# Kernel tuning notes

Hardware: AMD Instinct MI355X
Metric: run time of the kernel (lower is better)

Reference implementation:

```python
import jax, jax.numpy as jnp
import numpy as np

B, N, D_IN, D_OUT, E = 4, 50000, 128, 128, 800000


def setup_inputs() -> dict:
    key = jax.random.key(0)
    k_x, k_w, k_b, k_r, k_c, k_v = jax.random.split(key, 6)
    stdv = 1.0 / np.sqrt(D_OUT)
    x = jax.random.normal(k_x, (B, N, D_IN), dtype=jnp.float32)
    weight = jax.random.uniform(k_w, (D_IN, D_OUT), jnp.float32, -stdv, stdv)
    bias = jax.random.uniform(k_b, (D_OUT,), jnp.float32, -stdv, stdv)
    adj_rows = jax.random.randint(k_r, (E,), 0, N, dtype=jnp.int32)
    adj_cols = jax.random.randint(k_c, (E,), 0, N, dtype=jnp.int32)
    # positive edge weights (e.g. normalized adjacency values)
    adj_vals = jax.random.uniform(k_v, (E,), jnp.float32) * (1.0 / 16.0)
    edge_index = jnp.stack([adj_rows, adj_cols]).astype(jnp.int64)  # unused (pyg_builtin=False)
    return {"input": x, "weight": weight, "bias": bias,
            "adj_vals": adj_vals, "adj_rows": adj_rows, "adj_cols": adj_cols,
            "edge_index": edge_index}


def reference(input, weight, bias, adj_vals, adj_rows, adj_cols, edge_index):
    # support = input @ W : [B, N, D_OUT]
    support = jnp.einsum('bnd,df->bnf', input, weight)

    # node_repr = sparse adj (COO) @ support, batched == torch.sparse.mm path
    def agg(s):  # s: [N, D_OUT]
        msgs = adj_vals[:, None] * s[adj_cols]          # [E, D_OUT] gather
        return jax.ops.segment_sum(msgs, adj_rows, num_segments=N)  # scatter-add

    node_repr = jax.vmap(agg)(support) + bias           # [B, N, D_OUT]
    # net_norm='none' -> no norm; activation=relu; residual=False; dropout=0
    return jax.nn.relu(node_repr)
```

## Files before the change

### kernel.cpp

```cpp
#include <hip/hip_runtime.h>
#include <hip/hip_bf16.h>

#define BB 4
#define NN 50000
#define DIN 128
#define DOUT 128
#define EE 800000
#define TOTROWS (BB * NN)
#define LDA 136

#define NGB ((TOTROWS + 127) / 128)
#define MAXDEG 64
#define NAB (NN / 4)

typedef unsigned short u16;
typedef unsigned int u32;

using shortx8 = __attribute__((ext_vector_type(8))) short;
using ushortx4 = __attribute__((ext_vector_type(4))) unsigned short;
using ushortx8 = __attribute__((ext_vector_type(8))) unsigned short;
using floatx4 = __attribute__((ext_vector_type(4))) float;

__device__ __forceinline__ float b2f(u16 u) {
    u32 x = ((u32)u) << 16;
    float f;
    __builtin_memcpy(&f, &x, 4);
    return f;
}

__device__ __forceinline__ u16 f2b(float f) {
    u32 x;
    __builtin_memcpy(&x, &f, 4);
    u32 r = x + 0x7fffu + ((x >> 16) & 1u);
    return (u16)(r >> 16);
}

__device__ __forceinline__ long long pack_desc(int col, float val) {
    return (long long)(((unsigned long long)(u32)__float_as_int(val) << 32) |
                       (unsigned long long)(u32)col);
}

__global__ __launch_bounds__(256)
void k_prep(const u16* __restrict__ X, const void* __restrict__ Wv,
            const u16* __restrict__ Bs, const u16* __restrict__ V,
            int nx, int nw, int nb, int nv,
            int* __restrict__ flags, u16* __restrict__ Wt,
            int* __restrict__ cur) {
    __shared__ int cnt[4];
    const int tid = threadIdx.x;

    for (int i = (int)blockIdx.x * 256 + tid; i < NN; i += 65 * 256)
        cur[i] = 0;

    if (blockIdx.x == 0) {
        const int w = tid >> 6;
        const int l = tid & 63;
        if (tid < 4) cnt[tid] = 0;
        __syncthreads();
        const u16* p = (w == 0) ? X : (w == 1) ? (const u16*)Wv
                     : (w == 2) ? Bs : V;
        const int n  = (w == 0) ? nx : (w == 1) ? nw : (w == 2) ? nb : nv;
        int bad = 0;
        for (int k = 0; k < 4; ++k) {
            unsigned idx = 2u * (unsigned)(((unsigned long long)(l * 4 + k) *
                                            (unsigned)(n >> 1)) >> 8);
            u16 s = p[idx];
            unsigned e = (s >> 7) & 0xFF;
            bool ok = ((s & 0x7FFF) == 0) || (e >= 90 && e <= 141);
            bad += ok ? 0 : 1;
        }
        atomicAdd(&cnt[w], bad);
        __syncthreads();
        if (l == 0) flags[w] = (cnt[w] >= 77) ? 1 : 0;
    } else {
        if (tid == 0) cnt[0] = 0;
        __syncthreads();
        {
            unsigned idx = 2u * (unsigned)(((unsigned long long)tid *
                                            (unsigned)(nw >> 1)) >> 8);
            u16 s = ((const u16*)Wv)[idx];
            unsigned e = (s >> 7) & 0xFF;
            bool ok = ((s & 0x7FFF) == 0) || (e >= 90 && e <= 141);
            if (!ok) atomicAdd(&cnt[0], 1);
        }
        __syncthreads();
        const int wf32 = (cnt[0] >= 77) ? 1 : 0;
        int t = (int)(blockIdx.x - 1) * 256 + tid;
        int f = t >> 7, k = t & 127;
        size_t src = (size_t)k * DOUT + f;
        Wt[t] = wf32 ? f2b(((const float*)Wv)[src]) : ((const u16*)Wv)[src];
    }
}

__global__ __launch_bounds__(256, 3)
void k_gemmsc(const void* __restrict__ Xv, const u16* __restrict__ Wt,
              const int* __restrict__ flags, u16* __restrict__ sup,
              const int* __restrict__ rows, const int* __restrict__ cols,
              const void* __restrict__ valsv, int* __restrict__ cur,
              long long* __restrict__ epk) {
    __shared__ u16 lA[128 * LDA];

    const int tid = threadIdx.x;

    {
        int e0 = ((int)blockIdx.x * 256 + tid) * 2;
        if (e0 < EE) {
            const int vf32 = flags[3];
            int2 r2 = *(const int2*)(rows + e0);
            int2 c2 = *(const int2*)(cols + e0);
            float v0, v1;
            if (vf32) {
                float2 vv = *(const float2*)((const float*)valsv + e0);
                v0 = vv.x; v1 = vv.y;
            } else {
                u32 vv = *(const u32*)((const u16*)valsv + e0);
                v0 = b2f((u16)(vv & 0xFFFF));
                v1 = b2f((u16)(vv >> 16));
            }
            int s0 = atomicAdd(&cur[r2.x], 1);
            int s1 = atomicAdd(&cur[r2.y], 1);
            if (s0 < MAXDEG)
                epk[(size_t)r2.x * MAXDEG + s0] = pack_desc(c2.x, v0);
            if (s1 < MAXDEG)
                epk[(size_t)r2.y * MAXDEG + s1] = pack_desc(c2.y, v1);
        }
    }

    const int xf32 = flags[0];
    const int wid = tid >> 6;
    const int l   = tid & 63;
    const long rowBase = (long)blockIdx.x * 128;

    if (xf32) {
        const float* Xf = (const float*)Xv;
#pragma unroll
        for (int i = 0; i < 16; ++i) {
            int elem = i * 1024 + tid * 4;
            int row = elem >> 7, col = elem & 127;
            long gRow = rowBase + row;
            ushortx4 w4 = (ushortx4){0, 0, 0, 0};
            if (gRow < TOTROWS) {
                float4 v = *(const float4*)(Xf + gRow * DIN + col);
                w4[0] = f2b(v.x); w4[1] = f2b(v.y);
                w4[2] = f2b(v.z); w4[3] = f2b(v.w);
            }
            *(ushortx4*)&lA[row * LDA + col] = w4;
        }
    } else {
        const u16* X16 = (const u16*)Xv;
#pragma unroll
        for (int i = 0; i < 8; ++i) {
            int elem = i * 2048 + tid * 8;
            int row = elem >> 7, col = elem & 127;
            long gRow = rowBase + row;
            ushortx8 w8 = (ushortx8){0, 0, 0, 0, 0, 0, 0, 0};
            if (gRow < TOTROWS)
                w8 = *(const ushortx8*)(X16 + gRow * DIN + col);
            *(ushortx8*)&lA[row * LDA + col] = w8;
        }
    }

    const int wx = wid & 1;
    const int wy = wid >> 1;
    const int q8 = (l >> 4) * 8;
    const int lm = l & 15;

    shortx8 bf[16];
#pragma unroll
    for (int nt = 0; nt < 4; ++nt) {
        const size_t Frow = (size_t)(wx * 64 + nt * 16 + lm) * DIN;
#pragma unroll
        for (int c = 0; c < 4; ++c)
            bf[nt * 4 + c] = *(const shortx8*)(Wt + Frow + 32 * c + q8);
    }

    floatx4 acc[4][4];
#pragma unroll
    for (int mt = 0; mt < 4; ++mt)
#pragma unroll
        for (int nt = 0; nt < 4; ++nt)
            acc[mt][nt] = (floatx4){0.f, 0.f, 0.f, 0.f};

    __syncthreads();

    for (int c = 0; c < 4; ++c) {
        shortx8 af[4];
#pragma unroll
        for (int mt = 0; mt < 4; ++mt)
            af[mt] = *(const shortx8*)
                &lA[(size_t)(wy * 64 + mt * 16 + lm) * LDA + 32 * c + q8];
#pragma unroll
        for (int mt = 0; mt < 4; ++mt)
#pragma unroll
            for (int nt = 0; nt < 4; ++nt)
                acc[mt][nt] = __builtin_amdgcn_mfma_f32_16x16x32_bf16(
                    af[mt], bf[nt * 4 + c], acc[mt][nt], 0, 0, 0);
    }

    __syncthreads();
#pragma unroll
    for (int mt = 0; mt < 4; ++mt) {
#pragma unroll
        for (int reg = 0; reg < 4; ++reg) {
            int row = wy * 64 + mt * 16 + (l >> 4) * 4 + reg;
#pragma unroll
            for (int nt = 0; nt < 4; ++nt)
                lA[row * LDA + wx * 64 + nt * 16 + lm] = f2b(acc[mt][nt][reg]);
        }
    }
    __syncthreads();

#pragma unroll
    for (int i = 0; i < 8; ++i) {
        int elem = i * 2048 + tid * 8;
        int row = elem >> 7, col = elem & 127;
        long R = rowBase + row;
        if (R < TOTROWS) {
            int b = (int)(R / NN);
            int n = (int)(R % NN);
            ushortx8 v = *(const ushortx8*)&lA[row * LDA + col];
            *(ushortx8*)(sup + ((size_t)n * BB + b) * DOUT + col) = v;
        }
    }
}

__global__ __launch_bounds__(256)
void k_agg(const u16* __restrict__ sup, const int* __restrict__ cur,
           const long long* __restrict__ epk, const void* __restrict__ biasv,
           const int* __restrict__ flags, float* __restrict__ out) {
    int blk = blockIdx.x;
    const int pass = (blk >= NAB) ? 1 : 0;
    if (pass) blk -= NAB;
    const int wid = threadIdx.x >> 6;
    const int l   = threadIdx.x & 63;
    const int n = blk * 4 + wid;

    const int cnt = min(__builtin_amdgcn_readfirstlane(cur[n]), MAXDEG);

    float acc[4] = {0.f, 0.f, 0.f, 0.f};
    const int b  = l >> 4;
    const int f0 = pass * 64 + (l & 15) * 4;
    const int lofs = b * 128 + f0;

    int dx = 0, dy = 0;
    if (l < cnt) {
        long long dv = __builtin_nontemporal_load(
            epk + (size_t)n * MAXDEG + l);
        dx = (int)(dv & 0xFFFFFFFFLL);
        dy = (int)((unsigned long long)dv >> 32);
    }
    const int cnt8 = (cnt + 7) & ~7;
    for (int j = 0; j < cnt8; j += 8) {
        int   cs[8];
        float vs[8];
#pragma unroll
        for (int q = 0; q < 8; ++q) {
            cs[q] = __builtin_amdgcn_readlane(dx, j + q);
            vs[q] = __int_as_float(__builtin_amdgcn_readlane(dy, j + q));
        }
        ushortx4 sv[8];
#pragma unroll
        for (int q = 0; q < 8; ++q)
            sv[q] = *(const ushortx4*)(sup + (size_t)cs[q] * 512 + lofs);
#pragma unroll
        for (int q = 0; q < 8; ++q)
#pragma unroll
            for (int t = 0; t < 4; ++t)
                acc[t] += vs[q] * b2f(sv[q][t]);
    }

    float bb[4];
    if (flags[2]) {
        float4 bv = *(const float4*)((const float*)biasv + f0);
        bb[0] = bv.x; bb[1] = bv.y; bb[2] = bv.z; bb[3] = bv.w;
    } else {
        ushortx4 bv = *(const ushortx4*)((const u16*)biasv + f0);
#pragma unroll
        for (int t = 0; t < 4; ++t) bb[t] = b2f(bv[t]);
    }

    floatx4 r;
#pragma unroll
    for (int t = 0; t < 4; ++t) r[t] = fmaxf(acc[t] + bb[t], 0.f);

    float* op = out + ((size_t)b * NN + n) * DOUT + f0;
    __builtin_nontemporal_store(r, (floatx4*)op);
}

extern "C" void kernel_launch(void* const* d_in, const int* in_sizes, int n_in,
                              void* d_out, int out_size, void* d_ws, size_t ws_size,
                              hipStream_t stream) {
    const void* X    = d_in[0];
    const void* W    = d_in[1];
    const void* bias = d_in[2];
    const void* vals = d_in[3];
    const int* rows  = (const int*)d_in[4];
    const int* cols  = (const int*)d_in[5];
    float* out = (float*)d_out;

    char* base = (char*)d_ws;
    size_t o = 0;
    int* flags = (int*)(base + o); o += 64;
    int* cur = (int*)(base + o); o += (size_t)NN * 4;
    o = (o + 255) & ~(size_t)255;
    u16* Wt = (u16*)(base + o); o += (size_t)DIN * DOUT * 2;
    o = (o + 255) & ~(size_t)255;
    long long* epk = (long long*)(base + o);
    o += (size_t)NN * MAXDEG * 8;
    o = (o + 255) & ~(size_t)255;
    u16* sup = (u16*)(base + o); o += (size_t)BB * NN * DOUT * 2;
    (void)ws_size;

    k_prep<<<65, 256, 0, stream>>>((const u16*)X, W, (const u16*)bias,
                                   (const u16*)vals, in_sizes[0], in_sizes[1],
                                   in_sizes[2], in_sizes[3], flags, Wt, cur);
    k_gemmsc<<<NGB, 256, 0, stream>>>(X, Wt, flags, sup, rows, cols, vals,
                                      cur, epk);
    k_agg<<<2 * NAB, 256, 0, stream>>>(sup, cur, epk, bias, flags, out);
}
```

Baseline: 361.1 us.

## Swizzle GEMM LDS tile and add direct global-to-LDS load for bf16 input

Replaces the padded LDS tile (row stride 136) with an unpadded 128-wide tile whose 16-byte groups are XOR-swizzled by row to avoid bank conflicts, cutting LDS use so occupancy can rise to 4 blocks per CU. Adds a global_load_lds path that streams bf16 input rows straight into LDS with the swizzle applied, and moves the X tile load ahead of the edge-scatter work so the loads overlap it. The direct path only triggers for bf16 input on full blocks; fp32 input still converts through registers.

Measured after the change: 359.2 us. No clear change (-0.5%).

```diff
diff --git a/kernel.cpp b/kernel.cpp
--- a/kernel.cpp
+++ b/kernel.cpp
@@ -7,7 +7,6 @@
 #define DOUT 128
 #define EE 800000
 #define TOTROWS (BB * NN)
-#define LDA 136
 
 #define NGB ((TOTROWS + 127) / 128)
 #define MAXDEG 64
@@ -38,6 +37,10 @@
 __device__ __forceinline__ long long pack_desc(int col, float val) {
     return (long long)(((unsigned long long)(u32)__float_as_int(val) << 32) |
                        (unsigned long long)(u32)col);
+}
+
+__device__ __forceinline__ int lswz(int row, int g) {
+    return row * 256 + ((g ^ (row & 7)) << 4);
 }
 
 __global__ __launch_bounds__(256)
@@ -92,15 +95,63 @@
     }
 }
 
-__global__ __launch_bounds__(256, 3)
+__global__ __launch_bounds__(256, 4)
 void k_gemmsc(const void* __restrict__ Xv, const u16* __restrict__ Wt,
               const int* __restrict__ flags, u16* __restrict__ sup,
               const int* __restrict__ rows, const int* __restrict__ cols,
               const void* __restrict__ valsv, int* __restrict__ cur,
               long long* __restrict__ epk) {
-    __shared__ u16 lA[128 * LDA];
+    __shared__ u16 lA[128 * 128];
 
     const int tid = threadIdx.x;
+    const int wid = tid >> 6;
+    const int l   = tid & 63;
+    const long rowBase = (long)blockIdx.x * 128;
+    const int xf32 = flags[0];
+    const bool fullblk = (rowBase + 128 <= TOTROWS);
+
+    if (!xf32 && fullblk) {
+        const int rIG = l >> 4;
+        const int key = (wid * 4 + rIG) & 7;
+        const char* gp = (const char*)Xv
+                       + (size_t)(rowBase + wid * 4 + rIG) * (DIN * 2)
+                       + (((l & 15) ^ key) << 4);
+        char* lp = (char*)lA + (size_t)(wid * 4) * 256;
+#pragma unroll
+        for (int i = 0; i < 8; ++i) {
+            __builtin_amdgcn_global_load_lds(
+                (const __attribute__((address_space(1))) u32*)(gp + (size_t)i * 4096),
+                (__attribute__((address_space(3))) u32*)(lp + (size_t)i * 4096),
+                16, 0, 0);
+        }
+    } else if (xf32) {
+        const float* Xf = (const float*)Xv;
+#pragma unroll
+        for (int i = 0; i < 16; ++i) {
+            int elem = i * 1024 + tid * 4;
+            int row = elem >> 7, col = elem & 127;
+            long gRow = rowBase + row;
+            ushortx4 w4 = (ushortx4){0, 0, 0, 0};
+            if (gRow < TOTROWS) {
+                float4 v = *(const float4*)(Xf + gRow * DIN + col);
+                w4[0] = f2b(v.x); w4[1] = f2b(v.y);
+                w4[2] = f2b(v.z); w4[3] = f2b(v.w);
+            }
+            *(ushortx4*)((char*)lA + lswz(row, col >> 3) + (col & 7) * 2) = w4;
+        }
+    } else {
+        const u16* X16 = (const u16*)Xv;
+#pragma unroll
+        for (int i = 0; i < 8; ++i) {
+            int elem = i * 2048 + tid * 8;
+            int row = elem >> 7, col = elem & 127;
+            long gRow = rowBase + row;
+            ushortx8 w8 = (ushortx8){0, 0, 0, 0, 0, 0, 0, 0};
+            if (gRow < TOTROWS)
+                w8 = *(const ushortx8*)(X16 + gRow * DIN + col);
+            *(ushortx8*)((char*)lA + lswz(row, col >> 3)) = w8;
+        }
+    }
 
     {
         int e0 = ((int)blockIdx.x * 256 + tid) * 2;
@@ -126,44 +177,11 @@
         }
     }
 
-    const int xf32 = flags[0];
-    const int wid = tid >> 6;
-    const int l   = tid & 63;
-    const long rowBase = (long)blockIdx.x * 128;
-
-    if (xf32) {
-        const float* Xf = (const float*)Xv;
-#pragma unroll
-        for (int i = 0; i < 16; ++i) {
-            int elem = i * 1024 + tid * 4;
-            int row = elem >> 7, col = elem & 127;
-            long gRow = rowBase + row;
-            ushortx4 w4 = (ushortx4){0, 0, 0, 0};
-            if (gRow < TOTROWS) {
-                float4 v = *(const float4*)(Xf + gRow * DIN + col);
-                w4[0] = f2b(v.x); w4[1] = f2b(v.y);
-                w4[2] = f2b(v.z); w4[3] = f2b(v.w);
-            }
-            *(ushortx4*)&lA[row * LDA + col] = w4;
-        }
-    } else {
-        const u16* X16 = (const u16*)Xv;
-#pragma unroll
-        for (int i = 0; i < 8; ++i) {
-            int elem = i * 2048 + tid * 8;
-            int row = elem >> 7, col = elem & 127;
-            long gRow = rowBase + row;
-            ushortx8 w8 = (ushortx8){0, 0, 0, 0, 0, 0, 0, 0};
-            if (gRow < TOTROWS)
-                w8 = *(const ushortx8*)(X16 + gRow * DIN + col);
-            *(ushortx8*)&lA[row * LDA + col] = w8;
-        }
-    }
-
     const int wx = wid & 1;
     const int wy = wid >> 1;
     const int q8 = (l >> 4) * 8;
     const int lm = l & 15;
+    const int keyA = lm & 7;
 
     shortx8 bf[16];
 #pragma unroll
@@ -184,11 +202,13 @@
     __syncthreads();
 
     for (int c = 0; c < 4; ++c) {
+        const int G = (4 * c + (l >> 4)) ^ keyA;
         shortx8 af[4];
 #pragma unroll
-        for (int mt = 0; mt < 4; ++mt)
-            af[mt] = *(const shortx8*)
-                &lA[(size_t)(wy * 64 + mt * 16 + lm) * LDA + 32 * c + q8];
+        for (int mt = 0; mt < 4; ++mt) {
+            int row = wy * 64 + mt * 16 + lm;
+            af[mt] = *(const shortx8*)((const char*)lA + row * 256 + (G << 4));
+        }
 #pragma unroll
         for (int mt = 0; mt < 4; ++mt)
 #pragma unroll
@@ -204,8 +224,11 @@
         for (int reg = 0; reg < 4; ++reg) {
             int row = wy * 64 + mt * 16 + (l >> 4) * 4 + reg;
 #pragma unroll
-            for (int nt = 0; nt < 4; ++nt)
-                lA[row * LDA + wx * 64 + nt * 16 + lm] = f2b(acc[mt][nt][reg]);
+            for (int nt = 0; nt < 4; ++nt) {
+                int col = wx * 64 + nt * 16 + lm;
+                *(u16*)((char*)lA + lswz(row, col >> 3) + (col & 7) * 2) =
+                    f2b(acc[mt][nt][reg]);
+            }
         }
     }
     __syncthreads();
@@ -218,7 +241,7 @@
         if (R < TOTROWS) {
             int b = (int)(R / NN);
             int n = (int)(R % NN);
-            ushortx8 v = *(const ushortx8*)&lA[row * LDA + col];
+            ushortx8 v = *(const ushortx8*)((const char*)lA + lswz(row, col >> 3));
             *(ushortx8*)(sup + ((size_t)n * BB + b) * DOUT + col) = v;
         }
     }
```
